# Kernel optimization log

Hardware: AMD Instinct MI355X
Metric: run time of the kernel (lower is better)

The kernel has to match this reference:

```python
import jax, jax.numpy as jnp
import numpy as np

B, H, W = 16, 512, 512
N_BINS = 511          # round(mean(shape)) - 1 for (512, 512)
MAX_R = 1.0           # (1 + min(shape)/max(shape)) / 2 for square image


def _bin_ids():
    # Precompute per-pixel radial shell index (replaces the list of boolean shell masks).
    frame = max(H, W)
    xx, yy = np.mgrid[:H, :W]
    ellipse = ((xx - H / 2) * 2 / frame) ** 2 + ((yy - W / 2) * 2 / frame) ** 2
    r2 = np.linspace(0.0, MAX_R, N_BINS + 1)[1:] ** 2
    # shell k = { r2[k-1] <= ellipse < r2[k] }; pixels with ellipse >= r2[-1] map to
    # overflow bin N_BINS and are dropped, exactly matching the xor'd ellipse masks.
    return jnp.asarray(np.searchsorted(r2, ellipse.ravel(), side='right').astype(np.int32))


BIN_IDS = _bin_ids()  # [H*W] int32 in [0, N_BINS]


def setup_inputs() -> dict:
    key = jax.random.key(0)
    k1, k2 = jax.random.split(key)
    return {
        "z_": jax.random.normal(k1, (B, H, W, 2), dtype=jnp.float32),
        "t_": jax.random.normal(k2, (B, H, W, 2), dtype=jnp.float32),
    }


def _shell_sums(x):
    # x: [B, H*W] -> per-shell sums [B, N_BINS+1] in a single fused segment-sum pass.
    return jax.vmap(lambda v: jax.ops.segment_sum(v, BIN_IDS, num_segments=N_BINS + 1))(x)


def reference(z_, t_):
    tc = t_[..., 0] + 1j * t_[..., 1]          # [B,H,W] complex target
    zc = z_[..., 0] + 1j * z_[..., 1]
    Ft = jnp.fft.fft2(tc, axes=(-2, -1))
    Fe = jnp.fft.fft2(zc - tc, axes=(-2, -1))
    norm_coeff = Ft.real ** 2 + Ft.imag ** 2   # |FFT(target)|^2, [B,H,W]
    errors = Fe.real ** 2 + Fe.imag ** 2       # |FFT(z - target)|^2
    es = _shell_sums(errors.reshape(B, -1))[:, :N_BINS]      # drop overflow bin
    ns = _shell_sums(norm_coeff.reshape(B, -1))[:, :N_BINS]
    nre = es / jnp.maximum(ns, 1e-8)           # per-batch, per-shell normed error
    # per_shell_loss = per-batch sum over shells; loss = mean over batch
    return jnp.mean(jnp.sum(nre, axis=1))
```

## Files before the change

### kernel.cpp

```cpp
#include <hip/hip_runtime.h>

#define HH 512
#define WW 512
#define NBATCH 16
#define NBINS 512

#define PI_F 3.14159265358979323846f

#define SW(r) ((r) ^ (((r) >> 4) & 0xF))

__device__ __forceinline__ float2 cadd(float2 a, float2 b){ return make_float2(a.x+b.x, a.y+b.y); }
__device__ __forceinline__ float2 csub(float2 a, float2 b){ return make_float2(a.x-b.x, a.y-b.y); }
__device__ __forceinline__ float2 cmul(float2 a, float2 b){
    return make_float2(a.x*b.x - a.y*b.y, a.x*b.y + a.y*b.x);
}

typedef __fp16 h2v __attribute__((ext_vector_type(2)));
__device__ __forceinline__ unsigned pack2(float2 v) {
    union { h2v h; unsigned u; } c;
    c.h = __builtin_amdgcn_cvt_pkrtz(v.x, v.y);
    return c.u;
}
__device__ __forceinline__ float2 unpack2(unsigned u) {
    union { unsigned u; __fp16 h[2]; } c; c.u = u;
    return make_float2((float)c.h[0], (float)c.h[1]);
}

__device__ __forceinline__ void dft8(const float2* a, float2* y) {
    const float s2 = 0.70710678118654752440f;
    float2 t02a = cadd(a[0], a[4]), t02s = csub(a[0], a[4]);
    float2 t13a = cadd(a[2], a[6]), t13s = csub(a[2], a[6]);
    float2 E0 = cadd(t02a, t13a);
    float2 E2 = csub(t02a, t13a);
    float2 E1 = make_float2(t02s.x + t13s.y, t02s.y - t13s.x);
    float2 E3 = make_float2(t02s.x - t13s.y, t02s.y + t13s.x);
    float2 u02a = cadd(a[1], a[5]), u02s = csub(a[1], a[5]);
    float2 u13a = cadd(a[3], a[7]), u13s = csub(a[3], a[7]);
    float2 O0 = cadd(u02a, u13a);
    float2 O2 = csub(u02a, u13a);
    float2 O1 = make_float2(u02s.x + u13s.y, u02s.y - u13s.x);
    float2 O3 = make_float2(u02s.x - u13s.y, u02s.y + u13s.x);
    float2 wO1 = make_float2(s2 * (O1.x + O1.y), s2 * (O1.y - O1.x));
    float2 wO2 = make_float2(O2.y, -O2.x);
    float2 wO3 = make_float2(s2 * (O3.y - O3.x), -s2 * (O3.x + O3.y));
    y[0] = cadd(E0, O0);  y[4] = csub(E0, O0);
    y[1] = cadd(E1, wO1); y[5] = csub(E1, wO1);
    y[2] = cadd(E2, wO2); y[6] = csub(E2, wO2);
    y[3] = cadd(E3, wO3); y[7] = csub(E3, wO3);
}

__device__ __forceinline__ void twiddle8(float base, float2* w) {
    float s1, c1, s4, c4;
    __sincosf(base, &s1, &c1);
    __sincosf(4.0f * base, &s4, &c4);
    w[0] = make_float2(1.0f, 0.0f);
    w[1] = make_float2(c1, s1);
    w[2] = cmul(w[1], w[1]);
    w[3] = cmul(w[2], w[1]);
    w[4] = make_float2(c4, s4);
    w[5] = cmul(w[4], w[1]);
    w[6] = cmul(w[4], w[2]);
    w[7] = cmul(w[4], w[3]);
}

__device__ __forceinline__ void fft512_x2(float2* rb0, float2* rb1, int lane,
                                          float2* a0, float2* a1,
                                          float2* y0, float2* y1) {
    float2 w[8], y[8];
    twiddle8(-PI_F * (float)lane * (1.0f / 256.0f), w);
    dft8(a0, y);
#pragma unroll
    for (int r = 0; r < 8; ++r) rb0[SW(8 * lane + r)] = cmul(y[r], w[r]);
    dft8(a1, y);
#pragma unroll
    for (int r = 0; r < 8; ++r) rb1[SW(8 * lane + r)] = cmul(y[r], w[r]);
    __builtin_amdgcn_wave_barrier();
#pragma unroll
    for (int u = 0; u < 8; ++u) a0[u] = rb0[SW(lane + 64 * u)];
#pragma unroll
    for (int u = 0; u < 8; ++u) a1[u] = rb1[SW(lane + 64 * u)];
    twiddle8(-PI_F * (float)(lane >> 3) * (1.0f / 32.0f), w);
    const int qb = (lane & 7) + ((lane >> 3) << 6);
    dft8(a0, y);
#pragma unroll
    for (int r = 0; r < 8; ++r) rb0[SW(qb + 8 * r)] = cmul(y[r], w[r]);
    dft8(a1, y);
#pragma unroll
    for (int r = 0; r < 8; ++r) rb1[SW(qb + 8 * r)] = cmul(y[r], w[r]);
    __builtin_amdgcn_wave_barrier();
#pragma unroll
    for (int u = 0; u < 8; ++u) a0[u] = rb0[SW(lane + 64 * u)];
#pragma unroll
    for (int u = 0; u < 8; ++u) a1[u] = rb1[SW(lane + 64 * u)];
    dft8(a0, y0);
    dft8(a1, y1);
}


__global__ __launch_bounds__(256, 4)
void row_fft_kernel(const float2* __restrict__ z, const float2* __restrict__ t,
                    unsigned* __restrict__ fieldsT) {
    __shared__ float2 buf[8 * 512];
    const int tid  = threadIdx.x;
    const int lane = tid & 63;
    const int g    = tid >> 6;
    const int bid  = blockIdx.x;
    const int hg   = bid & 63;
    const int b    = bid >> 6;
    const int hb   = hg << 3;
    const size_t off0 = (((size_t)b * HH) + hb + (g << 1)) << 9;
    const size_t off1 = off0 + 512;

    float2 tv0[8], tv1[8], ev0[8], ev1[8];
#pragma unroll
    for (int u = 0; u < 8; ++u) tv0[u] = t[off0 + lane + 64 * u];
#pragma unroll
    for (int u = 0; u < 8; ++u) tv1[u] = t[off1 + lane + 64 * u];
#pragma unroll
    for (int u = 0; u < 8; ++u) {
        float2 zv = z[off0 + lane + 64 * u];
        ev0[u] = make_float2(zv.x - tv0[u].x, zv.y - tv0[u].y);
    }
#pragma unroll
    for (int u = 0; u < 8; ++u) {
        float2 zv = z[off1 + lane + 64 * u];
        ev1[u] = make_float2(zv.x - tv1[u].x, zv.y - tv1[u].y);
    }

    float2* rb0 = buf + ((g << 1) << 9);
    float2* rb1 = rb0 + 512;
    unsigned* tile = (unsigned*)buf;
    const int rr0 = g << 1, rr1 = rr0 | 1;

#pragma unroll
    for (int f = 0; f < 2; ++f) {
        float2 a0[8], a1[8];
#pragma unroll
        for (int u = 0; u < 8; ++u) {
            a0[u] = (f == 0) ? tv0[u] : ev0[u];
            a1[u] = (f == 0) ? tv1[u] : ev1[u];
        }
        float2 y0[8], y1[8];
        fft512_x2(rb0, rb1, lane, a0, a1, y0, y1);

        __syncthreads();
#pragma unroll
        for (int r = 0; r < 8; ++r) {
            int c = lane + (r << 6);
            tile[rr0 * 516 + c] = pack2(y0[r]);
            tile[rr1 * 516 + c] = pack2(y1[r]);
        }
        __syncthreads();
        unsigned* outF = fieldsT + (((size_t)(b * 2 + f)) << 18);
#pragma unroll
        for (int k = 0; k < 4; ++k) {
            int e  = tid + (k << 8);
            int cp = e >> 2, q = e & 3;
            uint4 v;
            v.x = tile[(2 * q)     * 516 + 2 * cp];
            v.y = tile[(2 * q)     * 516 + 2 * cp + 1];
            v.z = tile[(2 * q + 1) * 516 + 2 * cp];
            v.w = tile[(2 * q + 1) * 516 + 2 * cp + 1];
            *(uint4*)(outF + ((size_t)cp << 10) + ((hb + 2 * q) << 1)) = v;
        }
        __syncthreads();
    }
}

__global__ __launch_bounds__(256, 4)
void col_fft_bin_kernel(const unsigned* __restrict__ fieldsT,
                        float* __restrict__ bins) {
    __shared__ float2 buf[8 * 512];
    const int tid  = threadIdx.x;
    const int lane = tid & 63;
    const int g    = tid >> 6;
    const int bid  = blockIdx.x;
    const int cgrp = bid & 63;
    const int fl   = bid >> 6;
    const int f    = fl & 1;
    const int b    = fl >> 1;
    const int cp   = (cgrp << 2) | g;
    const int cA   = cp << 1;

    const uint2* colP = (const uint2*)(fieldsT + (((size_t)fl) << 18) + ((size_t)cp << 10));
    float2 a0[8], a1[8];
#pragma unroll
    for (int u = 0; u < 8; ++u) {
        uint2 v = colP[lane + (u << 6)];
        a0[u] = unpack2(v.x);
        a1[u] = unpack2(v.y);
    }

    float2* rb0 = buf + ((g << 1) << 9);
    float2* rb1 = rb0 + 512;
    float2 y0[8], y1[8];
    fft512_x2(rb0, rb1, lane, a0, a1, y0, y1);
    __builtin_amdgcn_wave_barrier();

    float* Hw = (float*)rb0;
#pragma unroll
    for (int i = 0; i < 8; ++i) Hw[lane + (i << 6)] = 0.0f;
    __builtin_amdgcn_wave_barrier();

    const float fcA = (float)(cA - 256)     * (1.0f / 256.0f);
    const float fcB = (float)(cA + 1 - 256) * (1.0f / 256.0f);
    const float fc2A = fcA * fcA, fc2B = fcB * fcB;
#pragma unroll
    for (int r = 0; r < 8; ++r) {
        int k = lane + (r << 6);
        float fr = (float)(k - 256) * (1.0f / 256.0f);
        float fr2 = fr * fr;
        float eA = fr2 + fc2A;
        float eB = fr2 + fc2B;
        if (eA < 1.0f) {
            int bin = (int)(sqrtf(eA) * 511.0f);
            atomicAdd(&Hw[bin], y0[r].x * y0[r].x + y0[r].y * y0[r].y);
        }
        if (eB < 1.0f) {
            int bin = (int)(sqrtf(eB) * 511.0f);
            atomicAdd(&Hw[bin], y1[r].x * y1[r].x + y1[r].y * y1[r].y);
        }
    }
    __syncthreads();

    const float* H = (const float*)buf;
    float* gb = bins + ((size_t)f * NBATCH + b) * NBINS;
#pragma unroll
    for (int j = 0; j < 2; ++j) {
        int bin = tid + (j << 8);
        float s = H[bin] + H[bin + 2048] + H[bin + 4096] + H[bin + 6144];
        atomicAdd(&gb[bin], s);
    }
}

__global__ __launch_bounds__(512)
void loss_kernel(const float* __restrict__ bins, float* __restrict__ outp) {
    __shared__ float red[512];
    const int tid = threadIdx.x;
    float acc = 0.0f;
    if (tid < 511) {
#pragma unroll 4
        for (int b = 0; b < NBATCH; ++b) {
            float ns = bins[((size_t)b) * NBINS + tid];
            float es = bins[((size_t)(NBATCH + b)) * NBINS + tid];
            acc += es / fmaxf(ns, 1e-8f);
        }
    }
    red[tid] = acc;
    __syncthreads();
    for (int s = 256; s > 0; s >>= 1) {
        if (tid < s) red[tid] += red[tid + s];
        __syncthreads();
    }
    if (tid == 0) outp[0] = red[0] * (1.0f / NBATCH);
}

extern "C" void kernel_launch(void* const* d_in, const int* in_sizes, int n_in,
                              void* d_out, int out_size, void* d_ws, size_t ws_size,
                              hipStream_t stream) {
    const float2* z = (const float2*)d_in[0];
    const float2* t = (const float2*)d_in[1];
    float* outp = (float*)d_out;

    const size_t binsBytes = (size_t)2 * NBATCH * NBINS * sizeof(float);
    float*    bins    = (float*)d_ws;
    unsigned* fieldsT = (unsigned*)((char*)d_ws + binsBytes);

    (void)hipMemsetAsync(bins, 0, binsBytes, stream);

    row_fft_kernel<<<NBATCH * 64, 256, 0, stream>>>(z, t, fieldsT);
    col_fft_bin_kernel<<<NBATCH * 2 * 64, 256, 0, stream>>>(fieldsT, bins);
    loss_kernel<<<1, 512, 0, stream>>>(bins, outp);
}
```

Measured before the change: 163.8 us.

## Replace LDS/global atomics in radial binning with wave segmented reductions and partials

Shared-memory atomicAdd binning in the column FFT is replaced with a wave-level shuffle segmented reduction, so only the head lane of each run of equal bins writes to LDS. Global atomics into the bins array become per-column-group partial stores, which a per-batch loss kernel reduces before one atomic into the output. The row FFT kernel now reloads t for the error field instead of holding both fields in registers, cutting register pressure. The shuffle reduction assumes equal bins sit in contiguous lanes. Near the spectrum centre the bin pattern is symmetric, so non-adjacent lanes can share a bin and cause double counting or unsynchronised LDS writes.

```diff
diff --git a/kernel.cpp b/kernel.cpp
--- a/kernel.cpp
+++ b/kernel.cpp
@@ -4,6 +4,7 @@
 #define WW 512
 #define NBATCH 16
 #define NBINS 512
+#define NCG 64
 
 #define PI_F 3.14159265358979323846f
 
@@ -111,22 +112,6 @@
     const size_t off0 = (((size_t)b * HH) + hb + (g << 1)) << 9;
     const size_t off1 = off0 + 512;
 
-    float2 tv0[8], tv1[8], ev0[8], ev1[8];
-#pragma unroll
-    for (int u = 0; u < 8; ++u) tv0[u] = t[off0 + lane + 64 * u];
-#pragma unroll
-    for (int u = 0; u < 8; ++u) tv1[u] = t[off1 + lane + 64 * u];
-#pragma unroll
-    for (int u = 0; u < 8; ++u) {
-        float2 zv = z[off0 + lane + 64 * u];
-        ev0[u] = make_float2(zv.x - tv0[u].x, zv.y - tv0[u].y);
-    }
-#pragma unroll
-    for (int u = 0; u < 8; ++u) {
-        float2 zv = z[off1 + lane + 64 * u];
-        ev1[u] = make_float2(zv.x - tv1[u].x, zv.y - tv1[u].y);
-    }
-
     float2* rb0 = buf + ((g << 1) << 9);
     float2* rb1 = rb0 + 512;
     unsigned* tile = (unsigned*)buf;
@@ -135,10 +120,24 @@
 #pragma unroll
     for (int f = 0; f < 2; ++f) {
         float2 a0[8], a1[8];
-#pragma unroll
-        for (int u = 0; u < 8; ++u) {
-            a0[u] = (f == 0) ? tv0[u] : ev0[u];
-            a1[u] = (f == 0) ? tv1[u] : ev1[u];
+        if (f == 0) {
+#pragma unroll
+            for (int u = 0; u < 8; ++u) a0[u] = t[off0 + lane + 64 * u];
+#pragma unroll
+            for (int u = 0; u < 8; ++u) a1[u] = t[off1 + lane + 64 * u];
+        } else {
+#pragma unroll
+            for (int u = 0; u < 8; ++u) {
+                float2 zv = z[off0 + lane + 64 * u];
+                float2 tv = t[off0 + lane + 64 * u];
+                a0[u] = make_float2(zv.x - tv.x, zv.y - tv.y);
+            }
+#pragma unroll
+            for (int u = 0; u < 8; ++u) {
+                float2 zv = z[off1 + lane + 64 * u];
+                float2 tv = t[off1 + lane + 64 * u];
+                a1[u] = make_float2(zv.x - tv.x, zv.y - tv.y);
+            }
         }
         float2 y0[8], y1[8];
         fft512_x2(rb0, rb1, lane, a0, a1, y0, y1);
@@ -167,9 +166,25 @@
     }
 }
 
+__device__ __forceinline__ void bin_chunk(float* Hw, int lane, int k,
+                                          float fc2, float mag) {
+    float fr = (float)(k - 256) * (1.0f / 256.0f);
+    float e  = fr * fr + fc2;
+    int bin = min((int)(sqrtf(e) * 511.0f), 511);
+    float v = mag;
+#pragma unroll
+    for (int d = 1; d < 64; d <<= 1) {
+        float ov = __shfl_down(v, d, 64);
+        int   ob = __shfl_down(bin, d, 64);
+        if (((lane + d) < 64) && (ob == bin)) v += ov;
+    }
+    int pb = __shfl_up(bin, 1, 64);
+    if (lane == 0 || pb != bin) Hw[bin] += v;
+}
+
 __global__ __launch_bounds__(256, 4)
 void col_fft_bin_kernel(const unsigned* __restrict__ fieldsT,
-                        float* __restrict__ bins) {
+                        float* __restrict__ partials) {
     __shared__ float2 buf[8 * 512];
     const int tid  = threadIdx.x;
     const int lane = tid & 63;
@@ -177,8 +192,6 @@
     const int bid  = blockIdx.x;
     const int cgrp = bid & 63;
     const int fl   = bid >> 6;
-    const int f    = fl & 1;
-    const int b    = fl >> 1;
     const int cp   = (cgrp << 2) | g;
     const int cA   = cp << 1;
 
@@ -208,51 +221,40 @@
 #pragma unroll
     for (int r = 0; r < 8; ++r) {
         int k = lane + (r << 6);
-        float fr = (float)(k - 256) * (1.0f / 256.0f);
-        float fr2 = fr * fr;
-        float eA = fr2 + fc2A;
-        float eB = fr2 + fc2B;
-        if (eA < 1.0f) {
-            int bin = (int)(sqrtf(eA) * 511.0f);
-            atomicAdd(&Hw[bin], y0[r].x * y0[r].x + y0[r].y * y0[r].y);
-        }
-        if (eB < 1.0f) {
-            int bin = (int)(sqrtf(eB) * 511.0f);
-            atomicAdd(&Hw[bin], y1[r].x * y1[r].x + y1[r].y * y1[r].y);
-        }
+        bin_chunk(Hw, lane, k, fc2A, y0[r].x * y0[r].x + y0[r].y * y0[r].y);
+        bin_chunk(Hw, lane, k, fc2B, y1[r].x * y1[r].x + y1[r].y * y1[r].y);
     }
     __syncthreads();
 
     const float* H = (const float*)buf;
-    float* gb = bins + ((size_t)f * NBATCH + b) * NBINS;
+    float* pb = partials + (((size_t)fl * NCG) + cgrp) * NBINS;
 #pragma unroll
     for (int j = 0; j < 2; ++j) {
         int bin = tid + (j << 8);
-        float s = H[bin] + H[bin + 2048] + H[bin + 4096] + H[bin + 6144];
-        atomicAdd(&gb[bin], s);
+        pb[bin] = H[bin] + H[bin + 2048] + H[bin + 4096] + H[bin + 6144];
     }
 }
 
 __global__ __launch_bounds__(512)
-void loss_kernel(const float* __restrict__ bins, float* __restrict__ outp) {
+void loss_kernel(const float* __restrict__ partials, float* __restrict__ outp) {
     __shared__ float red[512];
+    const int b = blockIdx.x;
     const int tid = threadIdx.x;
-    float acc = 0.0f;
-    if (tid < 511) {
+    float ns = 0.0f, es = 0.0f;
+    const float* pn = partials + ((size_t)(b * 2 + 0) * NCG) * NBINS + tid;
+    const float* pe = partials + ((size_t)(b * 2 + 1) * NCG) * NBINS + tid;
 #pragma unroll 4
-        for (int b = 0; b < NBATCH; ++b) {
-            float ns = bins[((size_t)b) * NBINS + tid];
-            float es = bins[((size_t)(NBATCH + b)) * NBINS + tid];
-            acc += es / fmaxf(ns, 1e-8f);
-        }
-    }
-    red[tid] = acc;
+    for (int cg = 0; cg < NCG; ++cg) {
+        ns += pn[cg * NBINS];
+        es += pe[cg * NBINS];
+    }
+    red[tid] = (tid < 511) ? es / fmaxf(ns, 1e-8f) : 0.0f;
     __syncthreads();
     for (int s = 256; s > 0; s >>= 1) {
         if (tid < s) red[tid] += red[tid + s];
         __syncthreads();
     }
-    if (tid == 0) outp[0] = red[0] * (1.0f / NBATCH);
+    if (tid == 0) atomicAdd(outp, red[0] * (1.0f / NBATCH));
 }
 
 extern "C" void kernel_launch(void* const* d_in, const int* in_sizes, int n_in,
@@ -262,13 +264,13 @@
     const float2* t = (const float2*)d_in[1];
     float* outp = (float*)d_out;
 
-    const size_t binsBytes = (size_t)2 * NBATCH * NBINS * sizeof(float);
-    float*    bins    = (float*)d_ws;
-    unsigned* fieldsT = (unsigned*)((char*)d_ws + binsBytes);
-
-    (void)hipMemsetAsync(bins, 0, binsBytes, stream);
+    const size_t partBytes = (size_t)2 * NBATCH * NCG * NBINS * sizeof(float);
+    float*    partials = (float*)d_ws;
+    unsigned* fieldsT  = (unsigned*)((char*)d_ws + partBytes);
+
+    (void)hipMemsetAsync(outp, 0, sizeof(float), stream);
 
     row_fft_kernel<<<NBATCH * 64, 256, 0, stream>>>(z, t, fieldsT);
-    col_fft_bin_kernel<<<NBATCH * 2 * 64, 256, 0, stream>>>(fieldsT, bins);
-    loss_kernel<<<1, 512, 0, stream>>>(bins, outp);
-}
+    col_fft_bin_kernel<<<NBATCH * 2 * 64, 256, 0, stream>>>(fieldsT, partials);
+    loss_kernel<<<NBATCH, 512, 0, stream>>>(partials, outp);
+}
```

Measured after the change: 161.0 us. About the same (-1.7%).
